# Kernel optimization log

Hardware: AMD Instinct MI355X
Metric: run time of the kernel (lower is better)

Reference implementation:

```python
import jax, jax.numpy as jnp
import numpy as np

B, S, D, H, N = 4, 2048, 512, 8, 64
HD = D // H  # head dim


def setup_inputs() -> dict:
    key = jax.random.key(0)
    ks = jax.random.split(key, 4)
    s = 0.02  # xavier-ish init scale
    return {
        "x": jax.random.normal(ks[0], (B, S, D), jnp.float32),
        "in_proj_w": jax.random.normal(ks[1], (3 * D, D), jnp.float32) * s,
        "in_proj_b": jnp.zeros((3 * D,), jnp.float32),
        "out_proj_w": jax.random.normal(ks[2], (D, D), jnp.float32) * s,
        "out_proj_b": jnp.zeros((D,), jnp.float32),
        "content_w": jax.random.normal(ks[3], (N, D), jnp.float32) * s,
        "content_b": jnp.zeros((N,), jnp.float32),
        "k_input": 16,
    }


def _fwd_core(x, in_proj_w, in_proj_b, out_proj_w, out_proj_b, content_w, content_b):
    # torch nn.MultiheadAttention (batch_first, eval/no dropout), self-attention
    qkv = jnp.einsum("bsd,ed->bse", x, in_proj_w) + in_proj_b  # [B,S,3D]
    q, k, v = jnp.split(qkv, 3, axis=-1)
    to_heads = lambda t: t.reshape(B, S, H, HD).transpose(0, 2, 1, 3)  # [B,H,S,hd]
    q, k, v = to_heads(q), to_heads(k), to_heads(v)
    scores = jnp.einsum("bhqd,bhkd->bhqk", q, k) / jnp.sqrt(jnp.float32(HD))
    attn = jax.nn.softmax(scores, axis=-1)  # [B,H,S,S] (need_weights=True path)
    ctx = jnp.einsum("bhqk,bhkd->bhqd", attn, v)
    ctx = ctx.transpose(0, 2, 1, 3).reshape(B, S, D)
    attended = jnp.einsum("bsd,ed->bse", ctx, out_proj_w) + out_proj_b  # [B,S,D]

    # content_to_neuron
    aff = jnp.einsum("bsd,nd->bsn", attended, content_w) + content_b  # [B,S,N]

    # position importance: mean over heads, sum over keys, normalize
    pos_imp = attn.mean(axis=1).sum(axis=2)  # [B,S]
    pos_imp = pos_imp / (pos_imp.sum(axis=1, keepdims=True) + 1e-8)

    weighted = (aff * pos_imp[..., None]).sum(axis=1)  # [B,N]
    final = 0.5 * weighted + 0.3 * aff.max(axis=1) + 0.2 * aff.mean(axis=1)
    probs = jax.nn.softmax(final, axis=-1)
    return final, probs, attended


def reference(x, in_proj_w, in_proj_b, out_proj_w, out_proj_b, content_w, content_b, k_input):
    final, probs, attended = _fwd_core(
        x, in_proj_w, in_proj_b, out_proj_w, out_proj_b, content_w, content_b
    )
    _, input_idx = jax.lax.top_k(final, k_input)  # [B,k]
    one_hot = jnp.zeros_like(probs).at[jnp.arange(B)[:, None], input_idx].set(1.0)
    # straight-through: value == one_hot, gradient flows through probs
    routing_weights = jax.lax.stop_gradient(one_hot - probs) + probs
    return input_idx, routing_weights, attended
```

## Files before the change

kernel.cpp:

```cpp
#include <hip/hip_runtime.h>
#include <hip/hip_bf16.h>

typedef unsigned short u16;
typedef unsigned int u32;
typedef __bf16 bf16x8 __attribute__((ext_vector_type(8)));
typedef u16 u16x8 __attribute__((ext_vector_type(8)));
typedef u16 u16x4 __attribute__((ext_vector_type(4)));
typedef float f32x4 __attribute__((ext_vector_type(4)));

__device__ __forceinline__ u16 f2bf(float f) {
  union { float f; unsigned u; } v; v.f = f;
  return (u16)((v.u + 0x7FFFu + ((v.u >> 16) & 1u)) >> 16);
}
__device__ __forceinline__ float bf2f(u16 h) {
  union { unsigned u; float f; } v; v.u = ((unsigned)h) << 16;
  return v.f;
}
__device__ __forceinline__ float asf(u32 u) {
  union { unsigned u; float f; } v; v.u = u; return v.f;
}
struct BfPair { u16 hi, lo; };
__device__ __forceinline__ BfPair split2(float f) {
  BfPair r;
  r.hi = f2bf(f);
  r.lo = f2bf(f - bf2f(r.hi));
  return r;
}
__device__ __forceinline__ bf16x8 as_bf16x8(u16x8 u) {
  union { u16x8 u; bf16x8 b; } v; v.u = u; return v.b;
}
__device__ __forceinline__ u32 cvt_pk(float a, float b) {
  u32 r;
  asm volatile("v_cvt_pk_bf16_f32 %0, %1, %2" : "=v"(r) : "v"(a), "v"(b));
  return r;
}

#define MFMA16(a, b, c) __builtin_amdgcn_mfma_f32_16x16x32_bf16((a), (b), (c), 0, 0, 0)

#define GLD16(gp, lp)                                                          \
  __builtin_amdgcn_global_load_lds(                                            \
      (const __attribute__((address_space(1))) void*)(gp),                     \
      (__attribute__((address_space(3))) void*)(lp), 16, 0, 0)

__global__ __launch_bounds__(256) void split_kernel(
    const float* __restrict__ src, u16* __restrict__ hi, u16* __restrict__ lo, int n4)
{
  int i = blockIdx.x * 256 + threadIdx.x;
  if (i >= n4) return;
  f32x4 v = ((const f32x4*)src)[i];
  u16x4 h, l;
  #pragma unroll
  for (int j = 0; j < 4; j++) { BfPair p = split2(v[j]); h[j] = p.hi; l[j] = p.lo; }
  ((u16x4*)hi)[i] = h;
  ((u16x4*)lo)[i] = l;
}

template<int OUT_PLANES>
__global__ __launch_bounds__(256, 3) void gemm_nt(
    const u16* __restrict__ Ah, const u16* __restrict__ Al,
    const u16* __restrict__ Bh, const u16* __restrict__ Bl,
    const float* __restrict__ bias,
    void* __restrict__ C0, void* __restrict__ C1,
    int M, int N, int K)
{
  __shared__ u16 Ash[128 * 32], Asl[128 * 32];
  __shared__ u16 Bsh[128 * 32], Bsl[128 * 32];
  const int t = threadIdx.x;
  const int lane = t & 63, w = t >> 6;
  const int l15 = lane & 15, g = lane >> 4;
  const int m0 = blockIdx.x * 128, n0 = blockIdx.y * 128;
  const int lrow = lane >> 2;
  const int lchunk = lane & 3;

  f32x4 acc[4][4] = {};

  for (int k0 = 0; k0 < K; k0 += 32) {
    __syncthreads();
    #pragma unroll
    for (int q = 0; q < 2; q++) {
      const int row = w * 32 + q * 16 + lrow;
      const int sw = lchunk ^ (row & 3) ^ ((row >> 2) & 3);
      const size_t ga = (size_t)(m0 + row) * K + k0 + sw * 8;
      const size_t gb = (size_t)(n0 + row) * K + k0 + sw * 8;
      const int ldsbase = (w * 32 + q * 16) * 32;
      GLD16(Ah + ga, &Ash[ldsbase]);
      GLD16(Al + ga, &Asl[ldsbase]);
      GLD16(Bh + gb, &Bsh[ldsbase]);
      GLD16(Bl + gb, &Bsl[ldsbase]);
    }
    __syncthreads();

    bf16x8 bh[4], bl[4];
    #pragma unroll
    for (int n = 0; n < 4; n++) {
      const int row = (w & 1) * 64 + n * 16 + l15;
      const int slot = g ^ (row & 3) ^ ((row >> 2) & 3);
      const int idx = row * 32 + slot * 8;
      bh[n] = *(const bf16x8*)&Bsh[idx];
      bl[n] = *(const bf16x8*)&Bsl[idx];
    }
    #pragma unroll
    for (int m = 0; m < 4; m++) {
      const int row = (w >> 1) * 64 + m * 16 + l15;
      const int slot = g ^ (row & 3) ^ ((row >> 2) & 3);
      const int idx = row * 32 + slot * 8;
      bf16x8 ah = *(const bf16x8*)&Ash[idx];
      bf16x8 al = *(const bf16x8*)&Asl[idx];
      #pragma unroll
      for (int n = 0; n < 4; n++) {
        acc[m][n] = MFMA16(ah, bh[n], acc[m][n]);
        acc[m][n] = MFMA16(ah, bl[n], acc[m][n]);
        acc[m][n] = MFMA16(al, bh[n], acc[m][n]);
      }
    }
  }

  const int r0 = m0 + (w >> 1) * 64;
  const int c0 = n0 + (w & 1) * 64;
  float bs[4];
  #pragma unroll
  for (int n = 0; n < 4; n++) bs[n] = bias[c0 + n * 16 + l15];
  #pragma unroll
  for (int m = 0; m < 4; m++)
    #pragma unroll
    for (int n = 0; n < 4; n++) {
      const int col = c0 + n * 16 + l15;
      #pragma unroll
      for (int r = 0; r < 4; r++) {
        float v = acc[m][n][r] + bs[n];
        size_t idx = (size_t)(r0 + m * 16 + g * 4 + r) * N + col;
        if (OUT_PLANES) {
          BfPair pp = split2(v);
          ((u16*)C0)[idx] = pp.hi;
          ((u16*)C1)[idx] = pp.lo;
        } else {
          ((float*)C0)[idx] = v;
        }
      }
    }
}

__global__ __launch_bounds__(512, 2) void attn_kernel(
    const u16* __restrict__ qkv_h, const u16* __restrict__ qkv_l,
    u16* __restrict__ ctx_h, u16* __restrict__ ctx_l)
{
  const int bh = blockIdx.x;
  const int b = bh >> 3, h = bh & 7;
  const int q0 = blockIdx.y * 256;
  const int t = threadIdx.x, lane = t & 63, w = t >> 6;
  const int l15 = lane & 15, g = lane >> 4;
  const int wh = w >> 2, wl = w & 3;

  __shared__ u16 Ksh[64 * 72];
  __shared__ u16 Vsh[64 * 72], Vsl[64 * 72];
  __shared__ u16 Ps[8][32 * 72];

  const size_t rowbase = (size_t)b * 2048;
  const float QSC = 0.125f * 1.44269504088896f;

  bf16x8 qbh[2][2], qbl[2][2];
  #pragma unroll
  for (int i = 0; i < 2; i++) {
    size_t qoff = (rowbase + q0 + wh * 128 + i * 64 + wl * 16 + l15) * 1536 + h * 64 + g * 8;
    #pragma unroll
    for (int kc = 0; kc < 2; kc++) {
      u16x8 uh = *(const u16x8*)(qkv_h + qoff + kc * 32);
      u16x8 ul = *(const u16x8*)(qkv_l + qoff + kc * 32);
      #pragma unroll
      for (int j = 0; j < 8; j++) {
        float v = (bf2f(uh[j]) + bf2f(ul[j])) * QSC;
        BfPair p = split2(v);
        uh[j] = p.hi; ul[j] = p.lo;
      }
      qbh[i][kc] = as_bf16x8(uh);
      qbl[i][kc] = as_bf16x8(ul);
    }
  }

  f32x4 oacc[2][4] = {};
  float l_q[2] = {0.f, 0.f};

  const int srow = t >> 3, scol = (t & 7) * 8;
  u16x8 skh, svh, svl;
  {
    size_t off = (rowbase + srow) * 1536 + h * 64 + scol;
    skh = *(const u16x8*)(qkv_h + off + 512);
    svh = *(const u16x8*)(qkv_h + off + 1024);
    svl = *(const u16x8*)(qkv_l + off + 1024);
  }

  for (int kt = 0; kt < 32; kt++) {
    __syncthreads();
    {
      *(u16x8*)&Ksh[srow * 72 + scol] = skh;
      int rk = (srow + scol) & 63;
      #pragma unroll
      for (int j = 0; j < 8; j++) {
        Vsh[(scol + j) * 72 + rk] = svh[j];
        Vsl[(scol + j) * 72 + rk] = svl[j];
      }
    }
    if (kt + 1 < 32) {
      size_t off = (rowbase + (kt + 1) * 64 + srow) * 1536 + h * 64 + scol;
      skh = *(const u16x8*)(qkv_h + off + 512);
      svh = *(const u16x8*)(qkv_h + off + 1024);
      svl = *(const u16x8*)(qkv_l + off + 1024);
    }
    __syncthreads();

    f32x4 sa0[4] = {}, sa1[4] = {};
    #pragma unroll
    for (int kc = 0; kc < 2; kc++) {
      #pragma unroll
      for (int cb = 0; cb < 4; cb++) {
        int ki = (cb * 16 + l15) * 72 + g * 8 + kc * 32;
        bf16x8 kh = *(const bf16x8*)&Ksh[ki];
        sa0[cb] = MFMA16(kh, qbh[0][kc], sa0[cb]);
        sa1[cb] = MFMA16(kh, qbh[1][kc], sa1[cb]);
        sa0[cb] = MFMA16(kh, qbl[0][kc], sa0[cb]);
        sa1[cb] = MFMA16(kh, qbl[1][kc], sa1[cb]);
      }
    }

    u32 hw[2][4][2];
    #pragma unroll
    for (int i = 0; i < 2; i++) {
      f32x4* sa = (i == 0) ? sa0 : sa1;
      float rs = 0.f;
      #pragma unroll
      for (int cb = 0; cb < 4; cb++) {
        #pragma unroll
        for (int r = 0; r < 4; r++) {
          float p = exp2f(sa[cb][r]);
          sa[cb][r] = p;
          rs += p;
        }
        hw[i][cb][0] = cvt_pk(sa[cb][0], sa[cb][1]);
        hw[i][cb][1] = cvt_pk(sa[cb][2], sa[cb][3]);
      }
      rs += __shfl_xor(rs, 16, 64);
      rs += __shfl_xor(rs, 32, 64);
      l_q[i] += rs;
    }

    #pragma unroll
    for (int i = 0; i < 2; i++)
      #pragma unroll
      for (int cb = 0; cb < 4; cb++) {
        u32* dst = (u32*)&Ps[w][(i * 16 + l15) * 72 + cb * 16 + g * 4];
        dst[0] = hw[i][cb][0]; dst[1] = hw[i][cb][1];
      }
    asm volatile("s_waitcnt lgkmcnt(0)" ::: "memory");
    __builtin_amdgcn_sched_barrier(0);
    bf16x8 pah[2][2];
    #pragma unroll
    for (int i = 0; i < 2; i++)
      #pragma unroll
      for (int kc = 0; kc < 2; kc++)
        pah[i][kc] = *(const bf16x8*)&Ps[w][(i * 16 + l15) * 72 + kc * 32 + g * 8];

    #pragma unroll
    for (int kc = 0; kc < 2; kc++) {
      #pragma unroll
      for (int cb = 0; cb < 4; cb++) {
        int d = cb * 16 + l15;
        int rk0 = (g * 8 + kc * 32 + (d & 56)) & 63;
        bf16x8 vbh = *(const bf16x8*)&Vsh[d * 72 + rk0];
        bf16x8 vbl = *(const bf16x8*)&Vsl[d * 72 + rk0];
        oacc[0][cb] = MFMA16(pah[0][kc], vbh, oacc[0][cb]);
        oacc[1][cb] = MFMA16(pah[1][kc], vbh, oacc[1][cb]);
        oacc[0][cb] = MFMA16(pah[0][kc], vbl, oacc[0][cb]);
        oacc[1][cb] = MFMA16(pah[1][kc], vbl, oacc[1][cb]);
      }
    }
  }

  #pragma unroll
  for (int i = 0; i < 2; i++)
    #pragma unroll
    for (int r = 0; r < 4; r++) {
      float lq = __shfl(l_q[i], g * 4 + r, 64);
      float inv = 1.0f / lq;
      int row = q0 + wh * 128 + i * 64 + wl * 16 + g * 4 + r;
      size_t base = (rowbase + row) * 512 + h * 64;
      #pragma unroll
      for (int cb = 0; cb < 4; cb++) {
        BfPair pp = split2(oacc[i][cb][r] * inv);
        ctx_h[base + cb * 16 + l15] = pp.hi;
        ctx_l[base + cb * 16 + l15] = pp.lo;
      }
    }
}

__global__ __launch_bounds__(256) void aff_reduce(
    const float* __restrict__ att, const float* __restrict__ cw,
    const float* __restrict__ cbias, float* __restrict__ psum, float* __restrict__ pmax)
{
  const int b = blockIdx.x, sb = blockIdx.y;
  const int t = threadIdx.x;
  const int n = t & 63, rg = t >> 6;
  __shared__ float cws[64 * 65];
  __shared__ float ats[32 * 65];
  __shared__ float reds[256], redm[256];

  float acc[8] = {};
  for (int kc = 0; kc < 8; kc++) {
    __syncthreads();
    #pragma unroll
    for (int i = 0; i < 4; i++) {
      int c = t + i * 256;
      int row = c >> 4, col = (c & 15) * 4;
      f32x4 v = *(const f32x4*)(cw + (size_t)row * 512 + kc * 64 + col);
      cws[row * 65 + col + 0] = v[0]; cws[row * 65 + col + 1] = v[1];
      cws[row * 65 + col + 2] = v[2]; cws[row * 65 + col + 3] = v[3];
    }
    #pragma unroll
    for (int i = 0; i < 2; i++) {
      int c = t + i * 256;
      int row = c >> 4, col = (c & 15) * 4;
      f32x4 v = *(const f32x4*)(att + ((size_t)b * 2048 + sb * 32 + row) * 512 + kc * 64 + col);
      ats[row * 65 + col + 0] = v[0]; ats[row * 65 + col + 1] = v[1];
      ats[row * 65 + col + 2] = v[2]; ats[row * 65 + col + 3] = v[3];
    }
    __syncthreads();
    for (int k = 0; k < 64; k++) {
      float c = cws[n * 65 + k];
      #pragma unroll
      for (int r = 0; r < 8; r++)
        acc[r] += ats[(rg * 8 + r) * 65 + k] * c;
    }
  }
  const float bn = cbias[n];
  float s = 0.f, m = -1e30f;
  #pragma unroll
  for (int r = 0; r < 8; r++) {
    float v = acc[r] + bn;
    s += v; m = fmaxf(m, v);
  }
  reds[t] = s; redm[t] = m;
  __syncthreads();
  if (t < 64) {
    float ss = reds[t] + reds[64 + t] + reds[128 + t] + reds[192 + t];
    float mm = fmaxf(fmaxf(redm[t], redm[64 + t]), fmaxf(redm[128 + t], redm[192 + t]));
    psum[((size_t)b * 64 + sb) * 64 + t] = ss;
    pmax[((size_t)b * 64 + sb) * 64 + t] = mm;
  }
}

__global__ void final_topk(const float* __restrict__ psum, const float* __restrict__ pmax,
                           float* __restrict__ out)
{
  __shared__ float fin[4][64];
  const int t = threadIdx.x;
  const int b = t >> 6, n = t & 63;
  float s = 0.f, m = -1e30f;
  for (int j = 0; j < 64; j++) {
    s += psum[((size_t)b * 64 + j) * 64 + n];
    m = fmaxf(m, pmax[((size_t)b * 64 + j) * 64 + n]);
  }
  const float mean = s * (1.0f / 2048.0f);
  fin[b][n] = 0.5f * mean + 0.3f * m + 0.2f * mean;
  __syncthreads();
  if (t < 4) {
    unsigned long long chosen = 0ull;
    for (int j = 0; j < 16; j++) {
      float best = -3e38f; int bi = 0;
      for (int nn = 0; nn < 64; nn++) {
        float v = fin[t][nn];
        if (!((chosen >> nn) & 1ull) && v > best) { best = v; bi = nn; }
      }
      chosen |= 1ull << bi;
      out[t * 16 + j] = (float)bi;
    }
    for (int nn = 0; nn < 64; nn++)
      out[64 + t * 64 + nn] = ((chosen >> nn) & 1ull) ? 1.0f : 0.0f;
  }
}

extern "C" void kernel_launch(void* const* d_in, const int* in_sizes, int n_in,
                              void* d_out, int out_size, void* d_ws, size_t ws_size,
                              hipStream_t stream) {
  const float* x    = (const float*)d_in[0];
  const float* win  = (const float*)d_in[1];
  const float* bin  = (const float*)d_in[2];
  const float* wout = (const float*)d_in[3];
  const float* bout = (const float*)d_in[4];
  const float* cw   = (const float*)d_in[5];
  const float* cbv  = (const float*)d_in[6];
  (void)in_sizes; (void)n_in; (void)ws_size; (void)out_size;

  float* out = (float*)d_out;
  char* ws = (char*)d_ws;
  u16*   qkv_h = (u16*)ws;
  u16*   qkv_l = (u16*)(ws + 25165824);
  u16*   ctx_h = (u16*)(ws + 50331648);
  u16*   ctx_l = (u16*)(ws + 58720256);
  float* psum  = (float*)(ws + 67108864);
  float* pmax  = (float*)(ws + 67174400);
  u16*   winh  = (u16*)(ws + 67239936);
  u16*   winl  = (u16*)(ws + 68812800);
  u16*   wouth = (u16*)(ws + 70385664);
  u16*   woutl = (u16*)(ws + 70909952);
  u16*   xh = ctx_h, *xl = ctx_l;
  float* attended = out + 320;

  split_kernel<<<4096, 256, 0, stream>>>(x, xh, xl, 1048576);
  split_kernel<<<768, 256, 0, stream>>>(win, winh, winl, 196608);
  split_kernel<<<256, 256, 0, stream>>>(wout, wouth, woutl, 65536);

  gemm_nt<1><<<dim3(64, 12), 256, 0, stream>>>(
      xh, xl, winh, winl, bin, qkv_h, qkv_l, 8192, 1536, 512);
  attn_kernel<<<dim3(32, 8), 512, 0, stream>>>(qkv_h, qkv_l, ctx_h, ctx_l);
  gemm_nt<0><<<dim3(64, 4), 256, 0, stream>>>(
      ctx_h, ctx_l, wouth, woutl, bout, attended, nullptr, 8192, 512, 512);
  aff_reduce<<<dim3(4, 64), 256, 0, stream>>>(attended, cw, cbv, psum, pmax);
  final_topk<<<1, 256, 0, stream>>>(psum, pmax, out);
}
```

Measured before the change: 243.9 us.

## Split attention over two key-range halves and merge partials in a combine kernel

The attention kernel now splits the key sequence into two halves along a new grid z-dimension. This doubles the block count so more of the machine's compute units can be kept busy. Each half writes unnormalized fp32 partial outputs and row sums, and a new combine kernel adds them, normalizes, and emits the bf16 hi/lo planes for the output projection. The cost is extra fp32 global memory traffic, one more launch, and workspace aliasing: partials go into the attended output and into the x split area, and the context is written into the qkv area.

```diff
diff --git a/kernel.cpp b/kernel.cpp
--- a/kernel.cpp
+++ b/kernel.cpp
@@ -142,11 +142,13 @@
 
 __global__ __launch_bounds__(512, 2) void attn_kernel(
     const u16* __restrict__ qkv_h, const u16* __restrict__ qkv_l,
-    u16* __restrict__ ctx_h, u16* __restrict__ ctx_l)
+    float* __restrict__ O0, float* __restrict__ O1,
+    float* __restrict__ l0, float* __restrict__ l1)
 {
   const int bh = blockIdx.x;
   const int b = bh >> 3, h = bh & 7;
   const int q0 = blockIdx.y * 256;
+  const int kt0 = blockIdx.z * 16;
   const int t = threadIdx.x, lane = t & 63, w = t >> 6;
   const int l15 = lane & 15, g = lane >> 4;
   const int wh = w >> 2, wl = w & 3;
@@ -183,13 +185,13 @@
   const int srow = t >> 3, scol = (t & 7) * 8;
   u16x8 skh, svh, svl;
   {
-    size_t off = (rowbase + srow) * 1536 + h * 64 + scol;
+    size_t off = (rowbase + kt0 * 64 + srow) * 1536 + h * 64 + scol;
     skh = *(const u16x8*)(qkv_h + off + 512);
     svh = *(const u16x8*)(qkv_h + off + 1024);
     svl = *(const u16x8*)(qkv_l + off + 1024);
   }
 
-  for (int kt = 0; kt < 32; kt++) {
+  for (int kt = kt0; kt < kt0 + 16; kt++) {
     __syncthreads();
     {
       *(u16x8*)&Ksh[srow * 72 + scol] = skh;
@@ -200,7 +202,7 @@
         Vsl[(scol + j) * 72 + rk] = svl[j];
       }
     }
-    if (kt + 1 < 32) {
+    if (kt + 1 < kt0 + 16) {
       size_t off = (rowbase + (kt + 1) * 64 + srow) * 1536 + h * 64 + scol;
       skh = *(const u16x8*)(qkv_h + off + 512);
       svh = *(const u16x8*)(qkv_h + off + 1024);
@@ -275,21 +277,50 @@
     }
   }
 
+  float* Op = (blockIdx.z == 0) ? O0 : O1;
+  float* lp = (blockIdx.z == 0) ? l0 : l1;
+  if (g == 0) {
+    #pragma unroll
+    for (int i = 0; i < 2; i++) {
+      int qrow = q0 + wh * 128 + i * 64 + wl * 16 + l15;
+      lp[(size_t)bh * 2048 + qrow] = l_q[i];
+    }
+  }
   #pragma unroll
   for (int i = 0; i < 2; i++)
     #pragma unroll
     for (int r = 0; r < 4; r++) {
-      float lq = __shfl(l_q[i], g * 4 + r, 64);
-      float inv = 1.0f / lq;
       int row = q0 + wh * 128 + i * 64 + wl * 16 + g * 4 + r;
       size_t base = (rowbase + row) * 512 + h * 64;
       #pragma unroll
-      for (int cb = 0; cb < 4; cb++) {
-        BfPair pp = split2(oacc[i][cb][r] * inv);
-        ctx_h[base + cb * 16 + l15] = pp.hi;
-        ctx_l[base + cb * 16 + l15] = pp.lo;
-      }
-    }
+      for (int cb = 0; cb < 4; cb++)
+        Op[base + cb * 16 + l15] = oacc[i][cb][r];
+    }
+}
+
+__global__ __launch_bounds__(256) void combine_kernel(
+    const float* __restrict__ O0, const float* __restrict__ O1,
+    const float* __restrict__ l0, const float* __restrict__ l1,
+    u16* __restrict__ ch, u16* __restrict__ cl)
+{
+  int i = blockIdx.x * 256 + threadIdx.x;
+  if (i >= 1048576) return;
+  f32x4 a = ((const f32x4*)O0)[i];
+  f32x4 c = ((const f32x4*)O1)[i];
+  int elem = i * 4;
+  int row = elem >> 9;
+  int d = elem & 511;
+  int bb = row >> 11, q = row & 2047, h = d >> 6;
+  size_t li = ((size_t)(bb * 8 + h)) * 2048 + q;
+  float inv = 1.0f / (l0[li] + l1[li]);
+  u16x4 hh, ll;
+  #pragma unroll
+  for (int j = 0; j < 4; j++) {
+    BfPair p = split2((a[j] + c[j]) * inv);
+    hh[j] = p.hi; ll[j] = p.lo;
+  }
+  ((u16x4*)ch)[i] = hh;
+  ((u16x4*)cl)[i] = ll;
 }
 
 __global__ __launch_bounds__(256) void aff_reduce(
@@ -393,16 +424,21 @@
   char* ws = (char*)d_ws;
   u16*   qkv_h = (u16*)ws;
   u16*   qkv_l = (u16*)(ws + 25165824);
-  u16*   ctx_h = (u16*)(ws + 50331648);
-  u16*   ctx_l = (u16*)(ws + 58720256);
   float* psum  = (float*)(ws + 67108864);
   float* pmax  = (float*)(ws + 67174400);
   u16*   winh  = (u16*)(ws + 67239936);
   u16*   winl  = (u16*)(ws + 68812800);
   u16*   wouth = (u16*)(ws + 70385664);
   u16*   woutl = (u16*)(ws + 70909952);
-  u16*   xh = ctx_h, *xl = ctx_l;
+  float* l0    = (float*)(ws + 71434240);
+  float* l1    = (float*)(ws + 71696384);
+  u16*   xh = (u16*)(ws + 50331648);
+  u16*   xl = (u16*)(ws + 58720256);
+  float* O1 = (float*)(ws + 50331648);
   float* attended = out + 320;
+  float* O0 = attended;
+  u16*   ctx2_h = qkv_h;
+  u16*   ctx2_l = qkv_h + 4194304;
 
   split_kernel<<<4096, 256, 0, stream>>>(x, xh, xl, 1048576);
   split_kernel<<<768, 256, 0, stream>>>(win, winh, winl, 196608);
@@ -410,9 +446,10 @@
 
   gemm_nt<1><<<dim3(64, 12), 256, 0, stream>>>(
       xh, xl, winh, winl, bin, qkv_h, qkv_l, 8192, 1536, 512);
-  attn_kernel<<<dim3(32, 8), 512, 0, stream>>>(qkv_h, qkv_l, ctx_h, ctx_l);
+  attn_kernel<<<dim3(32, 8, 2), 512, 0, stream>>>(qkv_h, qkv_l, O0, O1, l0, l1);
+  combine_kernel<<<4096, 256, 0, stream>>>(O0, O1, l0, l1, ctx2_h, ctx2_l);
   gemm_nt<0><<<dim3(64, 4), 256, 0, stream>>>(
-      ctx_h, ctx_l, wouth, woutl, bout, attended, nullptr, 8192, 512, 512);
+      ctx2_h, ctx2_l, wouth, woutl, bout, attended, nullptr, 8192, 512, 512);
   aff_reduce<<<dim3(4, 64), 256, 0, stream>>>(attended, cw, cbv, psum, pmax);
   final_topk<<<1, 256, 0, stream>>>(psum, pmax, out);
 }
```

After: 255.7 us. +4.8%, slower.
